# Kernel tuning notes

Hardware: AMD Instinct MI355X
Metric: run time of the kernel (lower is better)

The kernel has to match this reference:

```python
import jax, jax.numpy as jnp
import numpy as np

N_E = 16384
E_DIM = 256
SRC_DIM = 1024
BETA = 0.25


def setup_inputs() -> dict:
    key = jax.random.key(0)
    k_x, k_ew, k_eb, k_cb, k_dw, k_db = jax.random.split(key, 6)
    x = jax.random.normal(k_x, (16, 576, SRC_DIM), dtype=jnp.float32)
    # encoder Linear(source_dim -> embed_dim)
    enc_w = jax.random.normal(k_ew, (SRC_DIM, E_DIM), dtype=jnp.float32) / np.sqrt(SRC_DIM)
    enc_b = jax.random.normal(k_eb, (E_DIM,), dtype=jnp.float32) * 0.01
    # codebook initialized uniform(-1/n_e, 1/n_e) as in the torch module
    codebook = jax.random.uniform(k_cb, (N_E, E_DIM), dtype=jnp.float32, minval=-1.0 / N_E, maxval=1.0 / N_E)
    # decoder Linear(embed_dim -> source_dim)
    dec_w = jax.random.normal(k_dw, (E_DIM, SRC_DIM), dtype=jnp.float32) / np.sqrt(E_DIM)
    dec_b = jax.random.normal(k_db, (SRC_DIM,), dtype=jnp.float32) * 0.01
    return {"x": x, "enc_w": enc_w, "enc_b": enc_b, "codebook": codebook, "dec_w": dec_w, "dec_b": dec_b}


def reference(x, enc_w, enc_b, codebook, dec_w, dec_b):
    # encode: [B,S,src] -> [B,S,e]
    z = jnp.einsum('bsd,de->bse', x, enc_w) + enc_b
    # squared distances to all codebook entries: ||z||^2 + ||E||^2 - 2 z.E^T
    z2 = jnp.sum(z * z, axis=-1, keepdims=True)            # [B,S,1]
    e2 = jnp.sum(codebook * codebook, axis=-1)             # [n_e]
    cross = jnp.einsum('bse,ne->bsn', z, codebook)         # [B,S,n_e]
    d = z2 + e2 - 2.0 * cross
    idx = jnp.argmin(d, axis=-1)                           # [B,S] int
    z_q = codebook[idx]                                    # [B,S,e]
    sg = jax.lax.stop_gradient
    loss = BETA * jnp.mean((sg(z_q) - z) ** 2) + jnp.mean((z_q - sg(z)) ** 2)
    z_q_st = z + sg(z_q - z)                               # straight-through
    out = jnp.einsum('bse,ed->bsd', z_q_st, dec_w) + dec_b
    return (out, loss)
```

## Files before the change

### kernel.cpp

```cpp
#include <hip/hip_runtime.h>

typedef __bf16 bf16;
typedef __bf16 bf16x8 __attribute__((ext_vector_type(8)));
typedef float f32x4 __attribute__((ext_vector_type(4)));
typedef int i32x8 __attribute__((ext_vector_type(8)));
typedef unsigned int u32;
typedef unsigned char u8;

#define N_TOK 9216
#define SRC 1024
#define EDIM 256
#define NE 16384
#define GROUPS 16
#define GSIZE 1024
#define NBLK_LOSS 144
#define NEG_CB_SCALE -8192.0f
#define E2_SCALE 4096.0f
#define LOSS_DENOM 2359296.0f

__device__ __forceinline__ void async_load16(const void* g, void* l) {
  __builtin_amdgcn_global_load_lds(
      (__attribute__((address_space(1))) void*)(void*)(const_cast<void*>(g)),
      (__attribute__((address_space(3))) void*)l, 16, 0, 0);
}

__device__ __forceinline__ f32x4 mfma16(bf16x8 a, bf16x8 b, f32x4 c) {
  return __builtin_amdgcn_mfma_f32_16x16x32_bf16(a, b, c, 0, 0, 0);
}
__device__ __forceinline__ f32x4 mfma_mx(i32x8 a, i32x8 b, f32x4 c) {
  return __builtin_amdgcn_mfma_scale_f32_16x16x128_f8f6f4(
      a, b, c, 0, 0, 0, 0x7F7F7F7F, 0, 0x7F7F7F7F);
}

__global__ __launch_bounds__(256) void k_prep(const float* __restrict__ enc_w,
                                              const float* __restrict__ dec_w,
                                              const float* __restrict__ cb,
                                              bf16* __restrict__ enc_wT,
                                              bf16* __restrict__ dec_wT,
                                              u32* __restrict__ cbb8,
                                              float* __restrict__ e2s) {
  int b = blockIdx.x;
  if (b < 128) {
    __shared__ float T[64][65];
    const float* In;
    bf16* Out;
    int R, C, ti, tj;
    if (b < 64) {
      In = enc_w; Out = enc_wT; R = 1024; C = 256;
      ti = b & 15; tj = b >> 4;
    } else {
      int t2 = b - 64;
      In = dec_w; Out = dec_wT; R = 256; C = 1024;
      ti = t2 & 3; tj = t2 >> 2;
    }
    int c0 = threadIdx.x & 63, r0 = threadIdx.x >> 6;
#pragma unroll
    for (int i = 0; i < 16; i++) {
      int rr = r0 + i * 4;
      T[rr][c0] = In[(size_t)(ti * 64 + rr) * C + tj * 64 + c0];
    }
    __syncthreads();
#pragma unroll
    for (int i = 0; i < 16; i++) {
      int rr = r0 + i * 4;
      Out[(size_t)(tj * 64 + rr) * R + ti * 64 + c0] = (bf16)T[c0][rr];
    }
  } else {
    int row = (b - 128) * 4 + (threadIdx.x >> 6);
    int lane = threadIdx.x & 63;
    int slot = lane >> 2;
    int h = (slot & 8) | ((slot & 7) ^ (row & 7));
    int k0 = h * 16 + (lane & 3) * 4;
    float4 v = *(const float4*)(cb + (size_t)row * EDIM + k0);
    int pk = __builtin_amdgcn_cvt_pk_fp8_f32(v.x * NEG_CB_SCALE, v.y * NEG_CB_SCALE, 0, false);
    pk = __builtin_amdgcn_cvt_pk_fp8_f32(v.z * NEG_CB_SCALE, v.w * NEG_CB_SCALE, pk, true);
    cbb8[(size_t)row * 64 + lane] = (u32)pk;
    float sq = v.x * v.x + v.y * v.y + v.z * v.z + v.w * v.w;
#pragma unroll
    for (int off = 32; off; off >>= 1) sq += __shfl_xor(sq, off, 64);
    if (lane == 0) e2s[row] = E2_SCALE * (sq + 1.0f);
  }
}

__global__ __launch_bounds__(256) void k_enc(const float* __restrict__ x,
                                             const bf16* __restrict__ wT,
                                             const float* __restrict__ bias,
                                             u8* __restrict__ z8) {
  __shared__ __align__(16) bf16 As[2][64 * 32];
  __shared__ __align__(16) bf16 Bs[2][64 * 32];
  const int tid = threadIdx.x;
  const int wid = tid >> 6, lane = tid & 63;
  const int col = lane & 15, quad = lane >> 4;
  const int wm = (wid >> 1) * 32, wn = (wid & 1) * 32;
  const int bm = blockIdx.x * 64, bn = blockIdx.y * 64;
  f32x4 acc[2][2] = {};
  const int arow = tid >> 2, ags = tid & 3;

  float4 q0, q1;
  auto loadA = [&](int kc) {
    const float* p = x + (size_t)(bm + arow) * SRC + kc + ags * 8;
    q0 = *(const float4*)p;
    q1 = *(const float4*)(p + 4);
  };
  auto writeA = [&](int bb) {
    bf16x8 o = {(bf16)q0.x, (bf16)q0.y, (bf16)q0.z, (bf16)q0.w,
                (bf16)q1.x, (bf16)q1.y, (bf16)q1.z, (bf16)q1.w};
    *(bf16x8*)((char*)&As[bb][0] + (arow * 4 + (ags ^ (arow & 3))) * 16) = o;
  };
  auto stageB = [&](int kc, int bb) {
    int row = tid >> 2;
    int gg = (tid & 3) ^ (row & 3);
    async_load16(wT + (size_t)(bn + row) * SRC + kc + gg * 8,
                 (char*)&Bs[bb][0] + wid * 1024);
  };

  loadA(0);
  writeA(0);
  stageB(0, 0);
  for (int it = 0; it < 32; it++) {
    int cbuf = it & 1, nbuf = cbuf ^ 1;
    __syncthreads();
    if (it < 31) {
      loadA((it + 1) * 32);
      stageB((it + 1) * 32, nbuf);
    }
    bf16x8 afr[2], bfr[2];
#pragma unroll
    for (int t = 0; t < 2; t++) {
      int row = wm + t * 16 + col;
      afr[t] = *(const bf16x8*)((const char*)&As[cbuf][0] +
                                (row * 4 + (quad ^ (row & 3))) * 16);
    }
#pragma unroll
    for (int u = 0; u < 2; u++) {
      int row = wn + u * 16 + col;
      bfr[u] = *(const bf16x8*)((const char*)&Bs[cbuf][0] +
                                (row * 4 + (quad ^ (row & 3))) * 16);
    }
#pragma unroll
    for (int t = 0; t < 2; t++)
#pragma unroll
      for (int u = 0; u < 2; u++) acc[t][u] = mfma16(afr[t], bfr[u], acc[t][u]);
    if (it < 31) writeA(nbuf);
  }
#pragma unroll
  for (int u = 0; u < 2; u++) {
    int n = bn + wn + u * 16 + col;
    float bv = bias[n];
#pragma unroll
    for (int t = 0; t < 2; t++)
#pragma unroll
      for (int r = 0; r < 4; r++) {
        int m = bm + wm + t * 16 + quad * 4 + r;
        float v = acc[t][u][r] + bv;
        int pk = __builtin_amdgcn_cvt_pk_fp8_f32(v, v, 0, false);
        z8[(size_t)m * EDIM + n] = (u8)(pk & 0xFF);
      }
  }
}

__global__ __launch_bounds__(256, 3) void k_argmin(const u8* __restrict__ zb8,
                                                   const u8* __restrict__ cbb8,
                                                   const float* __restrict__ e2s,
                                                   float* __restrict__ pval,
                                                   int* __restrict__ pidx) {
  __shared__ __align__(16) u8 Cs[2 * 16384];
  __shared__ __align__(16) float Es[1024];
  const int tid = threadIdx.x;
  const int wid = tid >> 6, lane = tid & 63;
  const int col = lane & 15, quad = lane >> 4;
  const int g = blockIdx.y;
  const int tw = blockIdx.x * 192 + wid * 48;

  async_load16((const u8*)(e2s + g * GSIZE) + (size_t)tid * 16,
               (char*)Es + wid * 1024);

  i32x8 af[3][2];
#pragma unroll
  for (int t = 0; t < 3; t++)
#pragma unroll
    for (int m = 0; m < 2; m++) {
      const u8* p = zb8 + (size_t)(tw + t * 16 + col) * EDIM + m * 128 + quad * 32;
      int4 lo = *(const int4*)p;
      int4 hi = *(const int4*)(p + 16);
      af[t][m] = (i32x8){lo.x, lo.y, lo.z, lo.w, hi.x, hi.y, hi.z, hi.w};
    }

  u32 best[3][4];
#pragma unroll
  for (int t = 0; t < 3; t++)
#pragma unroll
    for (int r = 0; r < 4; r++) best[t][r] = 0xFFFFFFFFu;

  auto stage_load = [&](int st, int bb) {
    const u8* src = cbb8 + (size_t)(g * GSIZE + st * 64) * EDIM;
#pragma unroll
    for (int j = 0; j < 4; j++) {
      async_load16(src + (wid * 256 + j * 64 + lane) * 16,
                   (char*)Cs + bb * 16384 + wid * 4096 + j * 1024);
    }
  };

  stage_load(0, 0);
  asm volatile("s_waitcnt vmcnt(0)" ::: "memory");
  __builtin_amdgcn_s_barrier();

  const int r7 = col & 7;
  const int s0 = ((2 * quad) ^ r7) * 16;
  const int s1 = ((2 * quad + 1) ^ r7) * 16;

  for (int st = 0; st < 16; st++) {
    const char* bbase = (const char*)Cs + (st & 1) * 16384;
#pragma unroll
    for (int u = 0; u < 4; u++) {
      const int rb = (u * 16 + col) * 256;
      int4 a0 = *(const int4*)(bbase + rb + s0);
      int4 a1 = *(const int4*)(bbase + rb + s1);
      int4 b0 = *(const int4*)(bbase + rb + 128 + s0);
      int4 b1 = *(const int4*)(bbase + rb + 128 + s1);
      float ev = Es[st * 64 + u * 16 + col];
      if (u == 1 && st < 15) stage_load(st + 1, (st & 1) ^ 1);
      __builtin_amdgcn_s_barrier();
      asm volatile("s_waitcnt lgkmcnt(0)" ::: "memory");
      __builtin_amdgcn_sched_barrier(0);
      __builtin_amdgcn_s_setprio(1);
      i32x8 bm0 = (i32x8){a0.x, a0.y, a0.z, a0.w, a1.x, a1.y, a1.z, a1.w};
      i32x8 bm1 = (i32x8){b0.x, b0.y, b0.z, b0.w, b1.x, b1.y, b1.z, b1.w};
      f32x4 c0 = (f32x4){ev, ev, ev, ev};
      f32x4 c1 = c0, c2 = c0;
      c0 = mfma_mx(af[0][0], bm0, c0);
      c1 = mfma_mx(af[1][0], bm0, c1);
      c2 = mfma_mx(af[2][0], bm0, c2);
      c0 = mfma_mx(af[0][1], bm1, c0);
      c1 = mfma_mx(af[1][1], bm1, c1);
      c2 = mfma_mx(af[2][1], bm1, c2);
      __builtin_amdgcn_s_setprio(0);
      const u32 code = (u32)(st * 4 + u);
#pragma unroll
      for (int r = 0; r < 4; r++) {
        u32 k0 = (__float_as_uint(c0[r]) & 0xFFFFFFC0u) | code;
        u32 k1 = (__float_as_uint(c1[r]) & 0xFFFFFFC0u) | code;
        u32 k2 = (__float_as_uint(c2[r]) & 0xFFFFFFC0u) | code;
        best[0][r] = k0 < best[0][r] ? k0 : best[0][r];
        best[1][r] = k1 < best[1][r] ? k1 : best[1][r];
        best[2][r] = k2 < best[2][r] ? k2 : best[2][r];
      }
    }
    if (st < 15) asm volatile("s_waitcnt vmcnt(0)" ::: "memory");
    __builtin_amdgcn_s_barrier();
  }

#pragma unroll
  for (int t = 0; t < 3; t++)
#pragma unroll
    for (int r = 0; r < 4; r++) {
      u32 key = best[t][r];
      int cw = col;
#pragma unroll
      for (int off = 1; off < 16; off <<= 1) {
        u32 ok = (u32)__shfl_xor((int)key, off, 64);
        int oc = __shfl_xor(cw, off, 64);
        if (ok < key) { key = ok; cw = oc; }
      }
      if (col == 0) {
        int token = tw + t * 16 + quad * 4 + r;
        pval[token * GROUPS + g] = __uint_as_float(key & 0xFFFFFFC0u);
        pidx[token * GROUPS + g] = g * GSIZE + (int)(key & 63u) * 16 + cw;
      }
    }
}

__global__ __launch_bounds__(256) void k_dec(const float* __restrict__ cb,
                                             const float* __restrict__ pval,
                                             const int* __restrict__ pidx,
                                             const u8* __restrict__ zb8,
                                             const bf16* __restrict__ wT,
                                             const float* __restrict__ bias,
                                             float* __restrict__ out,
                                             float* __restrict__ lpart) {
  __shared__ __align__(16) bf16 As[2][64 * 32];
  __shared__ __align__(16) bf16 Bs[2][256 * 32];
  __shared__ int idxL[64];
  __shared__ float lsred[4];
  const int tid = threadIdx.x;
  const int wid = tid >> 6, lane = tid & 63;
  const int col = lane & 15, quad = lane >> 4;
  const int wm = (wid >> 1) * 32, wn = (wid & 1) * 128;
  const int bm = blockIdx.x * 64, bn = blockIdx.y * 256;
  const bool do_loss = (blockIdx.y == 0);

  {
    int tl = tid >> 2, j0 = tid & 3;
    float v = 3.4e38f;
    int idx = 0;
#pragma unroll
    for (int jj = 0; jj < 4; jj++) {
      int grp = j0 * 4 + jj;
      float ov = pval[(bm + tl) * GROUPS + grp];
      int oi = pidx[(bm + tl) * GROUPS + grp];
      if (ov < v || (ov == v && oi < idx)) { v = ov; idx = oi; }
    }
#pragma unroll
    for (int off = 1; off < 4; off <<= 1) {
      float ov = __shfl_xor(v, off, 64);
      int oi = __shfl_xor(idx, off, 64);
      if (ov < v || (ov == v && oi < idx)) { v = ov; idx = oi; }
    }
    if (j0 == 0) idxL[tl] = idx;
  }
  __syncthreads();

  const int arow = tid >> 2, ags = tid & 3;
  const int ridx = idxL[arow];
  float lacc = 0.f;
  f32x4 acc[2][8] = {};

  float4 q0, q1;
  auto loadA = [&](int kc) {
    const float* p = cb + (size_t)ridx * EDIM + kc + ags * 8;
    q0 = *(const float4*)p;
    q1 = *(const float4*)(p + 4);
    if (do_loss) {
      u32 zw0 = *(const u32*)(zb8 + (size_t)(bm + arow) * EDIM + kc + ags * 8);
      u32 zw1 = *(const u32*)(zb8 + (size_t)(bm + arow) * EDIM + kc + ags * 8 + 4);
      float d0 = q0.x - __builtin_amdgcn_cvt_f32_fp8(zw0, 0);
      float d1 = q0.y - __builtin_amdgcn_cvt_f32_fp8(zw0, 1);
      float d2 = q0.z - __builtin_amdgcn_cvt_f32_fp8(zw0, 2);
      float d3 = q0.w - __builtin_amdgcn_cvt_f32_fp8(zw0, 3);
      float d4 = q1.x - __builtin_amdgcn_cvt_f32_fp8(zw1, 0);
      float d5 = q1.y - __builtin_amdgcn_cvt_f32_fp8(zw1, 1);
      float d6 = q1.z - __builtin_amdgcn_cvt_f32_fp8(zw1, 2);
      float d7 = q1.w - __builtin_amdgcn_cvt_f32_fp8(zw1, 3);
      lacc += d0 * d0 + d1 * d1 + d2 * d2 + d3 * d3 +
              d4 * d4 + d5 * d5 + d6 * d6 + d7 * d7;
    }
  };
  auto writeA = [&](int bb) {
    bf16x8 o = {(bf16)q0.x, (bf16)q0.y, (bf16)q0.z, (bf16)q0.w,
                (bf16)q1.x, (bf16)q1.y, (bf16)q1.z, (bf16)q1.w};
    *(bf16x8*)((char*)&As[bb][0] + (arow * 4 + (ags ^ (arow & 3))) * 16) = o;
  };
  auto stageB = [&](int kc, int bb) {
#pragma unroll
    for (int j = 0; j < 4; j++) {
      int slot = wid * 256 + j * 64 + lane;
      int row = slot >> 2;
      int gg = (slot & 3) ^ (row & 3);
      async_load16(wT + (size_t)(bn + row) * EDIM + kc + gg * 8,
                   (char*)&Bs[bb][0] + wid * 4096 + j * 1024);
    }
  };

  loadA(0);
  writeA(0);
  stageB(0, 0);
  for (int it = 0; it < 8; it++) {
    int cbuf = it & 1, nbuf = cbuf ^ 1;
    __syncthreads();
    if (it < 7) {
      loadA((it + 1) * 32);
      stageB((it + 1) * 32, nbuf);
    }
    bf16x8 afr[2], bfr[8];
#pragma unroll
    for (int t = 0; t < 2; t++) {
      int row = wm + t * 16 + col;
      afr[t] = *(const bf16x8*)((const char*)&As[cbuf][0] +
                                (row * 4 + (quad ^ (row & 3))) * 16);
    }
#pragma unroll
    for (int u = 0; u < 8; u++) {
      int row = wn + u * 16 + col;
      bfr[u] = *(const bf16x8*)((const char*)&Bs[cbuf][0] +
                                (row * 4 + (quad ^ (row & 3))) * 16);
    }
#pragma unroll
    for (int t = 0; t < 2; t++)
#pragma unroll
      for (int u = 0; u < 8; u++) acc[t][u] = mfma16(afr[t], bfr[u], acc[t][u]);
    if (it < 7) writeA(nbuf);
  }

#pragma unroll
  for (int u = 0; u < 8; u++) {
    int n = bn + wn + u * 16 + col;
    float bv = bias[n];
#pragma unroll
    for (int t = 0; t < 2; t++)
#pragma unroll
      for (int r = 0; r < 4; r++) {
        int m = bm + wm + t * 16 + quad * 4 + r;
        out[(size_t)m * SRC + n] = acc[t][u][r] + bv;
      }
  }

  if (do_loss) {
#pragma unroll
    for (int off = 32; off; off >>= 1) lacc += __shfl_xor(lacc, off, 64);
    if (lane == 0) lsred[wid] = lacc;
    __syncthreads();
    if (tid == 0) lpart[blockIdx.x] = lsred[0] + lsred[1] + lsred[2] + lsred[3];
  }
}

__global__ __launch_bounds__(256) void k_loss(const float* __restrict__ lpart,
                                              float* __restrict__ outl) {
  float s = 0.f;
  if (threadIdx.x < NBLK_LOSS) s = lpart[threadIdx.x];
#pragma unroll
  for (int off = 32; off; off >>= 1) s += __shfl_xor(s, off, 64);
  __shared__ float ls[4];
  int wv = threadIdx.x >> 6;
  if ((threadIdx.x & 63) == 0) ls[wv] = s;
  __syncthreads();
  if (threadIdx.x == 0) *outl = 1.25f * (ls[0] + ls[1] + ls[2] + ls[3]) / LOSS_DENOM;
}

extern "C" void kernel_launch(void* const* d_in, const int* in_sizes, int n_in,
                              void* d_out, int out_size, void* d_ws, size_t ws_size,
                              hipStream_t stream) {
  const float* x = (const float*)d_in[0];
  const float* enc_w = (const float*)d_in[1];
  const float* enc_b = (const float*)d_in[2];
  const float* cb = (const float*)d_in[3];
  const float* dec_w = (const float*)d_in[4];
  const float* dec_b = (const float*)d_in[5];
  float* out = (float*)d_out;
  float* out_loss = out + (size_t)N_TOK * SRC;

  char* ws = (char*)d_ws;
  bf16* enc_wT = (bf16*)(ws + 0);
  bf16* dec_wT = (bf16*)(ws + 524288);
  u8* zb8 = (u8*)(ws + 1048576);
  u32* cbb8 = (u32*)(ws + 3407872);
  float* e2s = (float*)(ws + 7602176);
  float* pval = (float*)(ws + 7667712);
  int* pidx = (int*)(ws + 8257536);
  float* lpart = (float*)(ws + 8847360);

  k_prep<<<4224, 256, 0, stream>>>(enc_w, dec_w, cb, enc_wT, dec_wT, cbb8, e2s);
  k_enc<<<dim3(144, 4), 256, 0, stream>>>(x, enc_wT, enc_b, zb8);
  k_argmin<<<dim3(48, GROUPS), 256, 0, stream>>>(zb8, (const u8*)cbb8, e2s, pval, pidx);
  k_dec<<<dim3(144, 4), 256, 0, stream>>>(cb, pval, pidx, zb8, dec_wT, dec_b, out, lpart);
  k_loss<<<1, 256, 0, stream>>>(lpart, out_loss);
}
```

Before: 186.9 us.

## Stream codebook fragments straight from global into registers in argmin kernel

Removes the LDS double-buffered staging of the fp8 codebook in the argmin kernel. Each wave now loads its MFMA B fragments directly from global memory with a one-step register prefetch, and the per-wave barriers disappear. The prep kernel drops the XOR swizzle it applied to the codebook layout, and the grid is transposed so consecutive blocks share a codebook group for L2 reuse. This trades LDS traffic and synchronisation for redundant global/L2 loads, since all four waves now fetch the same codebook data, and exposes load latency to the limited prefetch depth.

```diff
diff --git a/kernel.cpp b/kernel.cpp
--- a/kernel.cpp
+++ b/kernel.cpp
@@ -68,10 +68,7 @@
   } else {
     int row = (b - 128) * 4 + (threadIdx.x >> 6);
     int lane = threadIdx.x & 63;
-    int slot = lane >> 2;
-    int h = (slot & 8) | ((slot & 7) ^ (row & 7));
-    int k0 = h * 16 + (lane & 3) * 4;
-    float4 v = *(const float4*)(cb + (size_t)row * EDIM + k0);
+    float4 v = *(const float4*)(cb + (size_t)row * EDIM + lane * 4);
     int pk = __builtin_amdgcn_cvt_pk_fp8_f32(v.x * NEG_CB_SCALE, v.y * NEG_CB_SCALE, 0, false);
     pk = __builtin_amdgcn_cvt_pk_fp8_f32(v.z * NEG_CB_SCALE, v.w * NEG_CB_SCALE, pk, true);
     cbb8[(size_t)row * 64 + lane] = (u32)pk;
@@ -164,13 +161,12 @@
                                                    const float* __restrict__ e2s,
                                                    float* __restrict__ pval,
                                                    int* __restrict__ pidx) {
-  __shared__ __align__(16) u8 Cs[2 * 16384];
   __shared__ __align__(16) float Es[1024];
   const int tid = threadIdx.x;
   const int wid = tid >> 6, lane = tid & 63;
   const int col = lane & 15, quad = lane >> 4;
-  const int g = blockIdx.y;
-  const int tw = blockIdx.x * 192 + wid * 48;
+  const int g = blockIdx.x;
+  const int tw = blockIdx.y * 192 + wid * 48;
 
   async_load16((const u8*)(e2s + g * GSIZE) + (size_t)tid * 16,
                (char*)Es + wid * 1024);
@@ -192,62 +188,53 @@
 #pragma unroll
     for (int r = 0; r < 4; r++) best[t][r] = 0xFFFFFFFFu;
 
-  auto stage_load = [&](int st, int bb) {
-    const u8* src = cbb8 + (size_t)(g * GSIZE + st * 64) * EDIM;
-#pragma unroll
-    for (int j = 0; j < 4; j++) {
-      async_load16(src + (wid * 256 + j * 64 + lane) * 16,
-                   (char*)Cs + bb * 16384 + wid * 4096 + j * 1024);
-    }
-  };
-
-  stage_load(0, 0);
-  asm volatile("s_waitcnt vmcnt(0)" ::: "memory");
-  __builtin_amdgcn_s_barrier();
-
-  const int r7 = col & 7;
-  const int s0 = ((2 * quad) ^ r7) * 16;
-  const int s1 = ((2 * quad + 1) ^ r7) * 16;
-
-  for (int st = 0; st < 16; st++) {
-    const char* bbase = (const char*)Cs + (st & 1) * 16384;
-#pragma unroll
-    for (int u = 0; u < 4; u++) {
-      const int rb = (u * 16 + col) * 256;
-      int4 a0 = *(const int4*)(bbase + rb + s0);
-      int4 a1 = *(const int4*)(bbase + rb + s1);
-      int4 b0 = *(const int4*)(bbase + rb + 128 + s0);
-      int4 b1 = *(const int4*)(bbase + rb + 128 + s1);
-      float ev = Es[st * 64 + u * 16 + col];
-      if (u == 1 && st < 15) stage_load(st + 1, (st & 1) ^ 1);
-      __builtin_amdgcn_s_barrier();
-      asm volatile("s_waitcnt lgkmcnt(0)" ::: "memory");
-      __builtin_amdgcn_sched_barrier(0);
-      __builtin_amdgcn_s_setprio(1);
-      i32x8 bm0 = (i32x8){a0.x, a0.y, a0.z, a0.w, a1.x, a1.y, a1.z, a1.w};
-      i32x8 bm1 = (i32x8){b0.x, b0.y, b0.z, b0.w, b1.x, b1.y, b1.z, b1.w};
-      f32x4 c0 = (f32x4){ev, ev, ev, ev};
-      f32x4 c1 = c0, c2 = c0;
-      c0 = mfma_mx(af[0][0], bm0, c0);
-      c1 = mfma_mx(af[1][0], bm0, c1);
-      c2 = mfma_mx(af[2][0], bm0, c2);
-      c0 = mfma_mx(af[0][1], bm1, c0);
-      c1 = mfma_mx(af[1][1], bm1, c1);
-      c2 = mfma_mx(af[2][1], bm1, c2);
-      __builtin_amdgcn_s_setprio(0);
-      const u32 code = (u32)(st * 4 + u);
-#pragma unroll
-      for (int r = 0; r < 4; r++) {
-        u32 k0 = (__float_as_uint(c0[r]) & 0xFFFFFFC0u) | code;
-        u32 k1 = (__float_as_uint(c1[r]) & 0xFFFFFFC0u) | code;
-        u32 k2 = (__float_as_uint(c2[r]) & 0xFFFFFFC0u) | code;
-        best[0][r] = k0 < best[0][r] ? k0 : best[0][r];
-        best[1][r] = k1 < best[1][r] ? k1 : best[1][r];
-        best[2][r] = k2 < best[2][r] ? k2 : best[2][r];
-      }
-    }
-    if (st < 15) asm volatile("s_waitcnt vmcnt(0)" ::: "memory");
-    __builtin_amdgcn_s_barrier();
+  __syncthreads();
+
+  const u8* cbase = cbb8 + ((size_t)g * GSIZE + col) * 256 + quad * 32;
+
+  int4 c0, c1, c2, c3;
+  {
+    const u8* rp = cbase;
+    c0 = *(const int4*)(rp);
+    c1 = *(const int4*)(rp + 16);
+    c2 = *(const int4*)(rp + 128);
+    c3 = *(const int4*)(rp + 144);
+  }
+
+#pragma unroll 4
+  for (int ph = 0; ph < 64; ph++) {
+    int4 n0, n1, n2, n3;
+    if (ph < 63) {
+      const u8* rp = cbase + (size_t)(ph + 1) * 4096;
+      n0 = *(const int4*)(rp);
+      n1 = *(const int4*)(rp + 16);
+      n2 = *(const int4*)(rp + 128);
+      n3 = *(const int4*)(rp + 144);
+    }
+    float ev = Es[ph * 16 + col];
+    i32x8 bm0 = (i32x8){c0.x, c0.y, c0.z, c0.w, c1.x, c1.y, c1.z, c1.w};
+    i32x8 bm1 = (i32x8){c2.x, c2.y, c2.z, c2.w, c3.x, c3.y, c3.z, c3.w};
+    f32x4 p0 = (f32x4){ev, ev, ev, ev};
+    f32x4 p1 = p0, p2 = p0;
+    __builtin_amdgcn_s_setprio(1);
+    p0 = mfma_mx(af[0][0], bm0, p0);
+    p1 = mfma_mx(af[1][0], bm0, p1);
+    p2 = mfma_mx(af[2][0], bm0, p2);
+    p0 = mfma_mx(af[0][1], bm1, p0);
+    p1 = mfma_mx(af[1][1], bm1, p1);
+    p2 = mfma_mx(af[2][1], bm1, p2);
+    __builtin_amdgcn_s_setprio(0);
+    const u32 code = (u32)ph;
+#pragma unroll
+    for (int r = 0; r < 4; r++) {
+      u32 k0 = (__float_as_uint(p0[r]) & 0xFFFFFFC0u) | code;
+      u32 k1 = (__float_as_uint(p1[r]) & 0xFFFFFFC0u) | code;
+      u32 k2 = (__float_as_uint(p2[r]) & 0xFFFFFFC0u) | code;
+      best[0][r] = k0 < best[0][r] ? k0 : best[0][r];
+      best[1][r] = k1 < best[1][r] ? k1 : best[1][r];
+      best[2][r] = k2 < best[2][r] ? k2 : best[2][r];
+    }
+    c0 = n0; c1 = n1; c2 = n2; c3 = n3;
   }
 
 #pragma unroll
@@ -440,7 +427,7 @@
 
   k_prep<<<4224, 256, 0, stream>>>(enc_w, dec_w, cb, enc_wT, dec_wT, cbb8, e2s);
   k_enc<<<dim3(144, 4), 256, 0, stream>>>(x, enc_wT, enc_b, zb8);
-  k_argmin<<<dim3(48, GROUPS), 256, 0, stream>>>(zb8, (const u8*)cbb8, e2s, pval, pidx);
+  k_argmin<<<dim3(GROUPS, 48), 256, 0, stream>>>(zb8, (const u8*)cbb8, e2s, pval, pidx);
   k_dec<<<dim3(144, 4), 256, 0, stream>>>(cb, pval, pidx, zb8, dec_wT, dec_b, out, lpart);
   k_loss<<<1, 256, 0, stream>>>(lpart, out_loss);
 }
```

New measurement: 243.6 us. +30.4%, slower.

## Split argmin codebook columns across wave pairs and cross-wave reduce in LDS

Applied to the files above, without the earlier changes.

Each wave in the argmin kernel now holds 96 tokens (six A fragments) and processes half of the codebook rows per stage. Each LDS B fragment read therefore feeds six MFMAs instead of three, which halves LDS read traffic per MFMA. The two waves covering the same tokens merge their partial minima through shared memory before writing results. The grid is transposed so group varies fastest, which changes how blocks share the token tile in cache. The cost is roughly double the VGPRs for A fragments and best keys, which risks occupancy at launch_bounds 3, plus an extra LDS reduction and barrier.

```diff
diff --git a/kernel.cpp b/kernel.cpp
--- a/kernel.cpp
+++ b/kernel.cpp
@@ -169,15 +169,17 @@
   const int tid = threadIdx.x;
   const int wid = tid >> 6, lane = tid & 63;
   const int col = lane & 15, quad = lane >> 4;
-  const int g = blockIdx.y;
-  const int tw = blockIdx.x * 192 + wid * 48;
+  const int g = blockIdx.x;
+  const int half = wid & 1;
+  const int ch = wid >> 1;
+  const int tw = blockIdx.y * 192 + half * 96;
 
   async_load16((const u8*)(e2s + g * GSIZE) + (size_t)tid * 16,
                (char*)Es + wid * 1024);
 
-  i32x8 af[3][2];
-#pragma unroll
-  for (int t = 0; t < 3; t++)
+  i32x8 af[6][2];
+#pragma unroll
+  for (int t = 0; t < 6; t++)
 #pragma unroll
     for (int m = 0; m < 2; m++) {
       const u8* p = zb8 + (size_t)(tw + t * 16 + col) * EDIM + m * 128 + quad * 32;
@@ -186,9 +188,9 @@
       af[t][m] = (i32x8){lo.x, lo.y, lo.z, lo.w, hi.x, hi.y, hi.z, hi.w};
     }
 
-  u32 best[3][4];
-#pragma unroll
-  for (int t = 0; t < 3; t++)
+  u32 best[6][4];
+#pragma unroll
+  for (int t = 0; t < 6; t++)
 #pragma unroll
     for (int r = 0; r < 4; r++) best[t][r] = 0xFFFFFFFFu;
 
@@ -209,49 +211,64 @@
   const int s0 = ((2 * quad) ^ r7) * 16;
   const int s1 = ((2 * quad + 1) ^ r7) * 16;
 
+#define MINUPD(t, pt)                                                 \
+  {                                                                   \
+    _Pragma("unroll") for (int r = 0; r < 4; r++) {                   \
+      u32 kk = (__float_as_uint(pt[r]) & 0xFFFFFFC0u) | code;         \
+      best[t][r] = kk < best[t][r] ? kk : best[t][r];                 \
+    }                                                                 \
+  }
+
   for (int st = 0; st < 16; st++) {
     const char* bbase = (const char*)Cs + (st & 1) * 16384;
 #pragma unroll
-    for (int u = 0; u < 4; u++) {
+    for (int j = 0; j < 2; j++) {
+      const int u = ch * 2 + j;
       const int rb = (u * 16 + col) * 256;
       int4 a0 = *(const int4*)(bbase + rb + s0);
       int4 a1 = *(const int4*)(bbase + rb + s1);
       int4 b0 = *(const int4*)(bbase + rb + 128 + s0);
       int4 b1 = *(const int4*)(bbase + rb + 128 + s1);
       float ev = Es[st * 64 + u * 16 + col];
-      if (u == 1 && st < 15) stage_load(st + 1, (st & 1) ^ 1);
+      if (j == 0 && st < 15) stage_load(st + 1, (st & 1) ^ 1);
       __builtin_amdgcn_s_barrier();
       asm volatile("s_waitcnt lgkmcnt(0)" ::: "memory");
       __builtin_amdgcn_sched_barrier(0);
       __builtin_amdgcn_s_setprio(1);
       i32x8 bm0 = (i32x8){a0.x, a0.y, a0.z, a0.w, a1.x, a1.y, a1.z, a1.w};
       i32x8 bm1 = (i32x8){b0.x, b0.y, b0.z, b0.w, b1.x, b1.y, b1.z, b1.w};
-      f32x4 c0 = (f32x4){ev, ev, ev, ev};
-      f32x4 c1 = c0, c2 = c0;
-      c0 = mfma_mx(af[0][0], bm0, c0);
-      c1 = mfma_mx(af[1][0], bm0, c1);
-      c2 = mfma_mx(af[2][0], bm0, c2);
-      c0 = mfma_mx(af[0][1], bm1, c0);
-      c1 = mfma_mx(af[1][1], bm1, c1);
-      c2 = mfma_mx(af[2][1], bm1, c2);
+      f32x4 p0 = (f32x4){ev, ev, ev, ev};
+      f32x4 p1 = p0, p2 = p0, p3 = p0, p4 = p0, p5 = p0;
+      p0 = mfma_mx(af[0][0], bm0, p0);
+      p1 = mfma_mx(af[1][0], bm0, p1);
+      p2 = mfma_mx(af[2][0], bm0, p2);
+      p3 = mfma_mx(af[3][0], bm0, p3);
+      p4 = mfma_mx(af[4][0], bm0, p4);
+      p5 = mfma_mx(af[5][0], bm0, p5);
+      p0 = mfma_mx(af[0][1], bm1, p0);
+      p1 = mfma_mx(af[1][1], bm1, p1);
+      p2 = mfma_mx(af[2][1], bm1, p2);
+      p3 = mfma_mx(af[3][1], bm1, p3);
+      p4 = mfma_mx(af[4][1], bm1, p4);
+      p5 = mfma_mx(af[5][1], bm1, p5);
       __builtin_amdgcn_s_setprio(0);
       const u32 code = (u32)(st * 4 + u);
-#pragma unroll
-      for (int r = 0; r < 4; r++) {
-        u32 k0 = (__float_as_uint(c0[r]) & 0xFFFFFFC0u) | code;
-        u32 k1 = (__float_as_uint(c1[r]) & 0xFFFFFFC0u) | code;
-        u32 k2 = (__float_as_uint(c2[r]) & 0xFFFFFFC0u) | code;
-        best[0][r] = k0 < best[0][r] ? k0 : best[0][r];
-        best[1][r] = k1 < best[1][r] ? k1 : best[1][r];
-        best[2][r] = k2 < best[2][r] ? k2 : best[2][r];
-      }
+      MINUPD(0, p0)
+      MINUPD(1, p1)
+      MINUPD(2, p2)
+      MINUPD(3, p3)
+      MINUPD(4, p4)
+      MINUPD(5, p5)
     }
     if (st < 15) asm volatile("s_waitcnt vmcnt(0)" ::: "memory");
     __builtin_amdgcn_s_barrier();
   }
-
-#pragma unroll
-  for (int t = 0; t < 3; t++)
+#undef MINUPD
+
+  u32* Rk = (u32*)Cs;
+  int* Rc = (int*)(Cs + 2048);
+#pragma unroll
+  for (int t = 0; t < 6; t++)
 #pragma unroll
     for (int r = 0; r < 4; r++) {
       u32 key = best[t][r];
@@ -263,11 +280,27 @@
         if (ok < key) { key = ok; cw = oc; }
       }
       if (col == 0) {
-        int token = tw + t * 16 + quad * 4 + r;
-        pval[token * GROUPS + g] = __uint_as_float(key & 0xFFFFFFC0u);
-        pidx[token * GROUPS + g] = g * GSIZE + (int)(key & 63u) * 16 + cw;
+        int ix = ((wid * 6 + t) * 4 + quad) * 4 + r;
+        Rk[ix] = key;
+        Rc[ix] = cw;
       }
     }
+  __syncthreads();
+  if (lane < 48) {
+    int item = ch * 48 + lane;
+    int t = item >> 4, rowin = item & 15;
+    int q2 = rowin >> 2, r = rowin & 3;
+    int ia = ((half * 6 + t) * 4 + q2) * 4 + r;
+    int ib = (((half + 2) * 6 + t) * 4 + q2) * 4 + r;
+    u32 ka = Rk[ia], kb = Rk[ib];
+    int ca = Rc[ia], cb2 = Rc[ib];
+    u32 k = ka;
+    int c = ca;
+    if (kb < ka) { k = kb; c = cb2; }
+    int token = blockIdx.y * 192 + half * 96 + item;
+    pval[token * GROUPS + g] = __uint_as_float(k & 0xFFFFFFC0u);
+    pidx[token * GROUPS + g] = g * GSIZE + (int)(k & 63u) * 16 + c;
+  }
 }
 
 __global__ __launch_bounds__(256) void k_dec(const float* __restrict__ cb,
@@ -440,7 +473,7 @@
 
   k_prep<<<4224, 256, 0, stream>>>(enc_w, dec_w, cb, enc_wT, dec_wT, cbb8, e2s);
   k_enc<<<dim3(144, 4), 256, 0, stream>>>(x, enc_wT, enc_b, zb8);
-  k_argmin<<<dim3(48, GROUPS), 256, 0, stream>>>(zb8, (const u8*)cbb8, e2s, pval, pidx);
+  k_argmin<<<dim3(GROUPS, 48), 256, 0, stream>>>(zb8, (const u8*)cbb8, e2s, pval, pidx);
   k_dec<<<dim3(144, 4), 256, 0, stream>>>(cb, pval, pidx, zb8, dec_wT, dec_b, out, lpart);
   k_loss<<<1, 256, 0, stream>>>(lpart, out_loss);
 }
```

Result: slower. 272.5 us (+45.8%).
